# Optimization experiments

Hardware: AMD Instinct MI355X
Metric: run time of the kernel (lower is better)

## Reference

```python
import jax, jax.numpy as jnp
import numpy as np
import math

D_MODEL = 1024
NUM_HEADS = 16
HEAD_DIM = D_MODEL // NUM_HEADS  # 64
THETA = 10000.0
BATCH = 2
SEQ = 2048


def setup_inputs() -> dict:
    key = jax.random.key(0)
    ks = jax.random.split(key, 5)
    scale = 0.02
    return {
        "in_features": jax.random.normal(ks[0], (BATCH, SEQ, D_MODEL), jnp.float32),
        "q_proj": jax.random.normal(ks[1], (D_MODEL, D_MODEL), jnp.float32) * scale,
        "k_proj": jax.random.normal(ks[2], (D_MODEL, D_MODEL), jnp.float32) * scale,
        "v_proj": jax.random.normal(ks[3], (D_MODEL, D_MODEL), jnp.float32) * scale,
        "o_proj": jax.random.normal(ks[4], (D_MODEL, D_MODEL), jnp.float32) * scale,
        "token_positions": jnp.arange(SEQ, dtype=jnp.int32),
    }


def _rope(x, token_positions):
    # x: [b, h, s, head_dim]; interleaved even/odd rotation
    half = HEAD_DIM // 2
    inv_freq = 1.0 / (THETA ** (2.0 * jnp.arange(half, dtype=x.dtype) / HEAD_DIM))
    angle = token_positions.astype(x.dtype)[:, None] * inv_freq[None, :]  # [s, half]
    cos, sin = jnp.cos(angle), jnp.sin(angle)
    x_e, x_o = x[..., ::2], x[..., 1::2]
    r_e = x_e * cos - x_o * sin
    r_o = x_e * sin + x_o * cos
    # interleave back: [..., s, half, 2] -> [..., s, head_dim]
    return jnp.stack([r_e, r_o], axis=-1).reshape(x.shape)


def reference(in_features, q_proj, k_proj, v_proj, o_proj, token_positions):
    b, s, _ = in_features.shape
    # projections: weight layout is [d_out, d_in]
    Q = jnp.einsum('bsd,kd->bsk', in_features, q_proj)
    K = jnp.einsum('bsd,kd->bsk', in_features, k_proj)
    V = jnp.einsum('bsd,kd->bsk', in_features, v_proj)
    # split heads: [b, h, s, head_dim]
    Q = Q.reshape(b, s, NUM_HEADS, HEAD_DIM).transpose(0, 2, 1, 3)
    K = K.reshape(b, s, NUM_HEADS, HEAD_DIM).transpose(0, 2, 1, 3)
    V = V.reshape(b, s, NUM_HEADS, HEAD_DIM).transpose(0, 2, 1, 3)
    Q = _rope(Q, token_positions)
    K = _rope(K, token_positions)
    scores = jnp.einsum('bhnd,bhmd->bhnm', Q, K) / math.sqrt(HEAD_DIM)
    causal = jnp.tril(jnp.ones((s, s), dtype=bool))  # [s, s]
    scores = jnp.where(causal[None, None], scores, -jnp.inf)
    attn = jax.nn.softmax(scores, axis=-1)
    out = jnp.einsum('bhnm,bhmd->bhnd', attn, V)
    out = out.transpose(0, 2, 1, 3).reshape(b, s, D_MODEL)
    return jnp.einsum('bsv,dv->bsd', out, o_proj)
```

## Files before the change

### kernel.cpp

```cpp
#include <hip/hip_runtime.h>
#include <hip/hip_bf16.h>

#define D_MODEL 1024
#define NHEAD   16
#define HDIM    64
#define SEQQ    2048
#define NBATCH  2
#define MROWS   (NBATCH * SEQQ)

typedef unsigned short u16;
typedef __attribute__((ext_vector_type(8))) short short8;
typedef __attribute__((ext_vector_type(4))) short bf16x4;
typedef __attribute__((ext_vector_type(4))) float floatx4;

__device__ __forceinline__ u16 f2b(float f) {
    union { __hip_bfloat16 h; u16 u; } cv;
    cv.h = __float2bfloat16(f);
    return cv.u;
}
__device__ __forceinline__ float b2f(u16 u) {
    return __uint_as_float(((unsigned int)u) << 16);
}
__device__ __forceinline__ short8 load8(const u16* p) {
    return *reinterpret_cast<const short8*>(p);
}
__device__ __forceinline__ bf16x4 load4v(const u16* p) {
    return *reinterpret_cast<const bf16x4*>(p);
}
__device__ __forceinline__ unsigned pack2(float lo, float hi) {
    return ((unsigned)f2b(hi) << 16) | (unsigned)f2b(lo);
}
__device__ __forceinline__ void async_cp16(const void* g, void* l) {
    __builtin_amdgcn_global_load_lds(
        (const __attribute__((address_space(1))) void*)g,
        (__attribute__((address_space(3))) void*)l, 16, 0, 0);
}

__global__ void cvt_all(const float* __restrict__ X,
                        const float* __restrict__ w0, const float* __restrict__ w1,
                        const float* __restrict__ w2, const float* __restrict__ w3,
                        const int* __restrict__ pos,
                        u16* __restrict__ xo,
                        u16* __restrict__ o0, u16* __restrict__ o1,
                        u16* __restrict__ o2, u16* __restrict__ o3,
                        float2* __restrict__ tab) {
    const int z = blockIdx.y;
    if (z == 8) {
        const int i = blockIdx.x * 256 + threadIdx.x;
        if (i < SEQQ * 32) {
            const int s = i >> 5, j = i & 31;
            const float p = (float)pos[s];
            const float inv = expf(-(float)j * (9.210340371976184f / 32.0f));
            float sn, cs;
            sincosf(p * inv, &sn, &cs);
            tab[i] = make_float2(cs, sn);
        }
        return;
    }
    const int n4 = (D_MODEL * D_MODEL) / 4;
    const float* in;
    u16* out;
    if (z < 4) { in = X + (size_t)z * n4 * 4;  out = xo + (size_t)z * n4 * 4; }
    else {
        in  = (z == 4) ? w0 : (z == 5) ? w1 : (z == 6) ? w2 : w3;
        out = (z == 4) ? o0 : (z == 5) ? o1 : (z == 6) ? o2 : o3;
    }
    const int i = blockIdx.x * 256 + threadIdx.x;
    float4 v = reinterpret_cast<const float4*>(in)[i];
    ushort4 o;
    o.x = f2b(v.x); o.y = f2b(v.y); o.z = f2b(v.z); o.w = f2b(v.w);
    reinterpret_cast<ushort4*>(out)[i] = o;
}

__global__ __launch_bounds__(256) void gemm_qkv(
    const u16* __restrict__ A,
    const u16* __restrict__ B0, const u16* __restrict__ B1, const u16* __restrict__ B2,
    u16* __restrict__ Qt, u16* __restrict__ Kt, u16* __restrict__ Vt,
    const float2* __restrict__ tab)
{
    const int K = D_MODEL;
    const int z = blockIdx.z;
    const u16* Bt = (z == 0) ? B0 : (z == 1 ? B1 : B2);

    __shared__ __attribute__((aligned(16))) u16 As[128 * 32];
    __shared__ __attribute__((aligned(16))) u16 Bs[128 * 32];

    const int tid  = threadIdx.x;
    const int w    = tid >> 6;
    const int lane = tid & 63;
    const int l15  = lane & 15;
    const int quad = lane >> 4;
    const int wm   = w >> 1, wn = w & 1;
    const int tm   = blockIdx.x * 128, tn = blockIdx.y * 128;

    floatx4 acc[4][4];
#pragma unroll
    for (int i = 0; i < 4; i++)
#pragma unroll
        for (int j = 0; j < 4; j++) {
            floatx4 zz = {0.f, 0.f, 0.f, 0.f};
            acc[i][j] = zz;
        }

    const int srow = lane >> 2;
    const int scol = (lane & 3) * 8;

    for (int k0 = 0; k0 < K; k0 += 32) {
#pragma unroll
        for (int ch = w; ch < 8; ch += 4) {
            async_cp16(A  + (size_t)(tm + ch * 16 + srow) * K + k0 + scol, &As[ch * 512]);
            async_cp16(Bt + (size_t)(tn + ch * 16 + srow) * K + k0 + scol, &Bs[ch * 512]);
        }
        __syncthreads();

        short8 af[4], bfr[4];
#pragma unroll
        for (int mi = 0; mi < 4; mi++)
            af[mi] = load8(&As[(wm * 64 + mi * 16 + l15) * 32 + quad * 8]);
#pragma unroll
        for (int ni = 0; ni < 4; ni++)
            bfr[ni] = load8(&Bs[(wn * 64 + ni * 16 + l15) * 32 + quad * 8]);
#pragma unroll
        for (int mi = 0; mi < 4; mi++)
#pragma unroll
            for (int ni = 0; ni < 4; ni++)
                acc[mi][ni] = __builtin_amdgcn_mfma_f32_16x16x32_bf16(af[mi], bfr[ni], acc[mi][ni], 0, 0, 0);
        __syncthreads();
    }

    if (z == 2) {
#pragma unroll
        for (int mi = 0; mi < 4; mi++) {
            const int r0 = tm + wm * 64 + mi * 16 + quad * 4;
            const int bb = r0 >> 11, s0 = r0 & (SEQQ - 1);
#pragma unroll
            for (int ni = 0; ni < 4; ni++) {
                const int colb = tn + wn * 64 + ni * 16 + l15;
                const int d = colb & 63, hh = colb >> 6;
                ushort4 pk;
                pk.x = f2b(acc[mi][ni][0]);
                pk.y = f2b(acc[mi][ni][1]);
                pk.z = f2b(acc[mi][ni][2]);
                pk.w = f2b(acc[mi][ni][3]);
                *reinterpret_cast<ushort4*>(
                    &Vt[(((size_t)(bb * NHEAD + hh)) * HDIM + d) * SEQQ + s0]) = pk;
            }
        }
    } else {
        const float qsc = (z == 0) ? 0.18033688011112042f : 1.0f;
        u16* Outp = (z == 0) ? Qt : Kt;
#pragma unroll
        for (int mi = 0; mi < 4; mi++) {
            const int r0 = tm + wm * 64 + mi * 16 + quad * 4;
#pragma unroll
            for (int ni = 0; ni < 4; ni++) {
                const int colb = tn + wn * 64 + ni * 16 + l15;
                const int d = colb & 63, hh = colb >> 6;
                const int j = d >> 1;
                const bool odd = (d & 1) != 0;
#pragma unroll
                for (int rg = 0; rg < 4; rg++) {
                    const int r = r0 + rg;
                    const int bb = r >> 11, s = r & (SEQQ - 1);
                    const float own = acc[mi][ni][rg];
                    const float oth = __shfl_xor(own, 1);
                    const float2 cs = tab[s * 32 + j];
                    const float xe = odd ? oth : own;
                    const float xo = odd ? own : oth;
                    const float res = odd ? (xe * cs.y + xo * cs.x)
                                          : (xe * cs.x - xo * cs.y);
                    Outp[(((size_t)(bb * NHEAD + hh)) * SEQQ + s) * HDIM + d] =
                        f2b(res * qsc);
                }
            }
        }
    }
}

__global__ __launch_bounds__(256, 4) void attn_kernel(
    const u16* __restrict__ Qt, const u16* __restrict__ Kt, const u16* __restrict__ Vt,
    u16* __restrict__ Out)
{
    const int bid = blockIdx.x;
    const int xcd = bid & 7;
    const int u   = bid >> 3;
    const int col = xcd * 4 + (u & 3);
    const int m   = u >> 2;
    int qsub;
    if      (m < 8)  qsub = 31 - m;
    else if (m < 16) qsub = m - 8;
    else if (m < 24) qsub = 39 - m;
    else             qsub = m - 16;
    const int h = col & (NHEAD - 1), b = col >> 4;

    const int tid = threadIdx.x, w = tid >> 6, lane = tid & 63;
    const int l15 = lane & 15, quad = lane >> 4;
    const size_t bh = (size_t)(b * NHEAD + h);
    const u16* Qh = Qt + bh * SEQQ * HDIM;
    const u16* Kh = Kt + bh * SEQQ * HDIM;
    const u16* Vh = Vt + bh * HDIM * SEQQ;

    __shared__ __attribute__((aligned(16))) u16 Ks[2][64 * 64];
    __shared__ __attribute__((aligned(16))) u16 Vs[2][64 * 64];

    short8 ones;
#pragma unroll
    for (int i = 0; i < 8; i++) ones[i] = (short)0x3F80;

    const int rr  = lane >> 3;
    const int swz = ((lane & 7) ^ rr) * 8;
    auto stage = [&](int buf, int tt) {
        const int k0s = tt * 64;
        async_cp16(Kh + (size_t)(k0s + w * 8 + rr) * HDIM + swz,       &Ks[buf][w * 512]);
        async_cp16(Kh + (size_t)(k0s + (w + 4) * 8 + rr) * HDIM + swz, &Ks[buf][(w + 4) * 512]);
        async_cp16(Vh + (size_t)(w * 8 + rr) * SEQQ + k0s + swz,       &Vs[buf][w * 512]);
        async_cp16(Vh + (size_t)((w + 4) * 8 + rr) * SEQQ + k0s + swz, &Vs[buf][(w + 4) * 512]);
    };

    const int s7  = l15 & 7;
    const int sw1 = ((quad)     ^ s7) * 8;
    const int sw2 = ((quad + 4) ^ s7) * 8;
    const int vo0 = (((quad >> 1)    ) ^ s7) * 8 + (quad & 1) * 4;
    const int vo1 = (((quad >> 1) + 2) ^ s7) * 8 + (quad & 1) * 4;
    const int vo2 = (((quad >> 1) + 4) ^ s7) * 8 + (quad & 1) * 4;
    const int vo3 = (((quad >> 1) + 6) ^ s7) * 8 + (quad & 1) * 4;

    const int q0w   = qsub * 64 + w * 16;
    const int tmaxp = qsub;

    short8 qf[2];
#pragma unroll
    for (int kk = 0; kk < 2; kk++)
        qf[kk] = load8(&Qh[(size_t)(q0w + l15) * HDIM + kk * 32 + quad * 8]);

    floatx4 O[4];
    floatx4 l_acc = {0.f, 0.f, 0.f, 0.f};
#pragma unroll
    for (int c = 0; c < 4; c++) { floatx4 zz = {0.f, 0.f, 0.f, 0.f}; O[c] = zz; }

    stage(0, 0);

    for (int t = 0; t <= tmaxp; ++t) {
        asm volatile("s_waitcnt vmcnt(0)" ::: "memory");
        __builtin_amdgcn_s_barrier();
        if (t < tmaxp) stage((t + 1) & 1, t + 1);

        const u16* KsB = &Ks[t & 1][0];
        const u16* VsB = &Vs[t & 1][0];
        const int k0 = t * 64;

        floatx4 S[4];
#pragma unroll
        for (int c = 0; c < 4; c++) {
            const int rowb = (c * 16 + l15) * 64;
            floatx4 zz = {0.f, 0.f, 0.f, 0.f};
            S[c] = __builtin_amdgcn_mfma_f32_16x16x32_bf16(load8(&KsB[rowb + sw1]), qf[0], zz,   0, 0, 0);
            S[c] = __builtin_amdgcn_mfma_f32_16x16x32_bf16(load8(&KsB[rowb + sw2]), qf[1], S[c], 0, 0, 0);
        }

        if (t == tmaxp) {
            const int q = q0w + l15;
#pragma unroll
            for (int c = 0; c < 4; c++)
#pragma unroll
                for (int r = 0; r < 4; r++)
                    if (k0 + c * 16 + quad * 4 + r > q) S[c][r] = -1e30f;
        }

#pragma unroll
        for (int c = 0; c < 4; c++)
#pragma unroll
            for (int r = 0; r < 4; r++)
                S[c][r] = __builtin_amdgcn_exp2f(S[c][r]);

        union { short8 v; unsigned u[4]; } pf0, pf1;
        pf0.u[0] = pack2(S[0][0], S[0][1]);
        pf0.u[1] = pack2(S[0][2], S[0][3]);
        pf0.u[2] = pack2(S[1][0], S[1][1]);
        pf0.u[3] = pack2(S[1][2], S[1][3]);
        pf1.u[0] = pack2(S[2][0], S[2][1]);
        pf1.u[1] = pack2(S[2][2], S[2][3]);
        pf1.u[2] = pack2(S[3][0], S[3][1]);
        pf1.u[3] = pack2(S[3][2], S[3][3]);

        l_acc = __builtin_amdgcn_mfma_f32_16x16x32_bf16(pf0.v, ones, l_acc, 0, 0, 0);
        l_acc = __builtin_amdgcn_mfma_f32_16x16x32_bf16(pf1.v, ones, l_acc, 0, 0, 0);

#pragma unroll
        for (int c2 = 0; c2 < 4; c2++) {
            const int rowb = (c2 * 16 + l15) * 64;
            bf16x4 a0 = load4v(&VsB[rowb + vo0]);
            bf16x4 a1 = load4v(&VsB[rowb + vo1]);
            bf16x4 a2 = load4v(&VsB[rowb + vo2]);
            bf16x4 a3 = load4v(&VsB[rowb + vo3]);
            short8 v0 = __builtin_shufflevector(a0, a1, 0, 1, 2, 3, 4, 5, 6, 7);
            short8 v1 = __builtin_shufflevector(a2, a3, 0, 1, 2, 3, 4, 5, 6, 7);
            O[c2] = __builtin_amdgcn_mfma_f32_16x16x32_bf16(pf0.v, v0, O[c2], 0, 0, 0);
            O[c2] = __builtin_amdgcn_mfma_f32_16x16x32_bf16(pf1.v, v1, O[c2], 0, 0, 0);
        }
    }

    float inv_l[4];
#pragma unroll
    for (int r = 0; r < 4; r++) inv_l[r] = 1.0f / l_acc[r];

#pragma unroll
    for (int c2 = 0; c2 < 4; c2++)
#pragma unroll
        for (int r = 0; r < 4; r++) {
            const int q    = q0w + quad * 4 + r;
            const int colo = h * HDIM + c2 * 16 + l15;
            Out[(size_t)(b * SEQQ + q) * D_MODEL + colo] = f2b(O[c2][r] * inv_l[r]);
        }
}

__global__ __launch_bounds__(256) void gemm_o(
    const u16* __restrict__ A, const u16* __restrict__ Bt, float* __restrict__ C)
{
    const int K = D_MODEL, N = D_MODEL;
    __shared__ __attribute__((aligned(16))) u16 As[64 * 32];
    __shared__ __attribute__((aligned(16))) u16 Bs[128 * 32];

    const int tid  = threadIdx.x;
    const int w    = tid >> 6;
    const int lane = tid & 63;
    const int l15  = lane & 15;
    const int quad = lane >> 4;
    const int wm   = w >> 1, wn = w & 1;
    const int tm   = blockIdx.x * 64, tn = blockIdx.y * 128;

    floatx4 acc[2][4];
#pragma unroll
    for (int i = 0; i < 2; i++)
#pragma unroll
        for (int j = 0; j < 4; j++) {
            floatx4 z = {0.f, 0.f, 0.f, 0.f};
            acc[i][j] = z;
        }

    const int srow = lane >> 2;
    const int scol = (lane & 3) * 8;

    for (int k0 = 0; k0 < K; k0 += 32) {
#pragma unroll
        for (int ch = w; ch < 12; ch += 4) {
            if (ch < 4) async_cp16(A  + (size_t)(tm + ch * 16 + srow) * K + k0 + scol, &As[ch * 512]);
            else        async_cp16(Bt + (size_t)(tn + (ch - 4) * 16 + srow) * K + k0 + scol, &Bs[(ch - 4) * 512]);
        }
        __syncthreads();

        short8 af[2], bfr[4];
#pragma unroll
        for (int mi = 0; mi < 2; mi++)
            af[mi] = load8(&As[(wm * 32 + mi * 16 + l15) * 32 + quad * 8]);
#pragma unroll
        for (int ni = 0; ni < 4; ni++)
            bfr[ni] = load8(&Bs[(wn * 64 + ni * 16 + l15) * 32 + quad * 8]);
#pragma unroll
        for (int mi = 0; mi < 2; mi++)
#pragma unroll
            for (int ni = 0; ni < 4; ni++)
                acc[mi][ni] = __builtin_amdgcn_mfma_f32_16x16x32_bf16(af[mi], bfr[ni], acc[mi][ni], 0, 0, 0);
        __syncthreads();
    }

#pragma unroll
    for (int mi = 0; mi < 2; mi++)
#pragma unroll
        for (int ni = 0; ni < 4; ni++)
#pragma unroll
            for (int rg = 0; rg < 4; rg++) {
                int row = tm + wm * 32 + mi * 16 + quad * 4 + rg;
                int col = tn + wn * 64 + ni * 16 + l15;
                C[(size_t)row * N + col] = acc[mi][ni][rg];
            }
}

extern "C" void kernel_launch(void* const* d_in, const int* in_sizes, int n_in,
                              void* d_out, int out_size, void* d_ws, size_t ws_size,
                              hipStream_t stream)
{
    const float* X  = (const float*)d_in[0];
    const float* Wq = (const float*)d_in[1];
    const float* Wk = (const float*)d_in[2];
    const float* Wv = (const float*)d_in[3];
    const float* Wo = (const float*)d_in[4];
    const int* tpos = (const int*)d_in[5];
    float* out = (float*)d_out;
    char* ws = (char*)d_ws;

    const size_t MB = (size_t)1 << 20;
    u16*    Xb  = (u16*)(ws + 0);
    u16*    WqB = (u16*)(ws + 8 * MB);
    u16*    WkB = (u16*)(ws + 10 * MB);
    u16*    WvB = (u16*)(ws + 12 * MB);
    u16*    WoB = (u16*)(ws + 14 * MB);
    float2* tab = (float2*)(ws + 16 * MB);
    u16*    Qt  = (u16*)(ws + 24 * MB);
    u16*    Kt  = (u16*)(ws + 32 * MB);
    u16*    Vt  = (u16*)(ws + 40 * MB);
    u16*   AOut = (u16*)(ws + 48 * MB);

    cvt_all<<<dim3(1024, 9), 256, 0, stream>>>(X, Wq, Wk, Wv, Wo, tpos,
                                               Xb, WqB, WkB, WvB, WoB, tab);

    gemm_qkv<<<dim3(32, 8, 3), 256, 0, stream>>>(Xb, WqB, WkB, WvB,
                                                 Qt, Kt, Vt, tab);
    attn_kernel<<<dim3(1024, 1, 1), 256, 0, stream>>>(Qt, Kt, Vt, AOut);
    gemm_o<<<dim3(64, 8), 256, 0, stream>>>(AOut, WoB, out);
}
```

Measured before the change: 190.0 us.

## Double-buffer GEMM LDS tiles and de-interleave Q/K weights for vectorized RoPE

Both projection GEMMs get double-buffered LDS staging, so the async global-to-LDS copy of the next K tile overlaps the MFMA work on the current tile, using raw barriers and vmcnt waits. The Q/K weight rows are permuted during the bf16 conversion so even and odd RoPE dimensions land in separate column halves. This lets the epilogue pair accumulators within a thread instead of using cross-lane shuffles. The cos/sin table is transposed to [j][s] so each thread can read consecutive positions with float4 loads. The cost is twice the LDS per block, which may lower occupancy, plus the Q/K stores in the epilogue become scattered 2-byte writes.

Result: faster. 186.3 us (-2.0%).

```diff
diff --git a/kernel.cpp b/kernel.cpp
--- a/kernel.cpp
+++ b/kernel.cpp
@@ -45,10 +45,10 @@
                         u16* __restrict__ o2, u16* __restrict__ o3,
                         float2* __restrict__ tab) {
     const int z = blockIdx.y;
+    const int i = blockIdx.x * 256 + threadIdx.x;
     if (z == 8) {
-        const int i = blockIdx.x * 256 + threadIdx.x;
         if (i < SEQQ * 32) {
-            const int s = i >> 5, j = i & 31;
+            const int j = i >> 11, s = i & (SEQQ - 1);
             const float p = (float)pos[s];
             const float inv = expf(-(float)j * (9.210340371976184f / 32.0f));
             float sn, cs;
@@ -65,8 +65,14 @@
         in  = (z == 4) ? w0 : (z == 5) ? w1 : (z == 6) ? w2 : w3;
         out = (z == 4) ? o0 : (z == 5) ? o1 : (z == 6) ? o2 : o3;
     }
-    const int i = blockIdx.x * 256 + threadIdx.x;
-    float4 v = reinterpret_cast<const float4*>(in)[i];
+    int src = i;
+    if (z == 4 || z == 5) {
+        const int orow = i >> 8;
+        const int g    = i & 255;
+        const int irow = (orow & ~63) | (((orow & 31) << 1) | ((orow >> 5) & 1));
+        src = irow * 256 + g;
+    }
+    float4 v = reinterpret_cast<const float4*>(in)[src];
     ushort4 o;
     o.x = f2b(v.x); o.y = f2b(v.y); o.z = f2b(v.z); o.w = f2b(v.w);
     reinterpret_cast<ushort4*>(out)[i] = o;
@@ -82,8 +88,8 @@
     const int z = blockIdx.z;
     const u16* Bt = (z == 0) ? B0 : (z == 1 ? B1 : B2);
 
-    __shared__ __attribute__((aligned(16))) u16 As[128 * 32];
-    __shared__ __attribute__((aligned(16))) u16 Bs[128 * 32];
+    __shared__ __attribute__((aligned(16))) u16 As[2][128 * 32];
+    __shared__ __attribute__((aligned(16))) u16 Bs[2][128 * 32];
 
     const int tid  = threadIdx.x;
     const int w    = tid >> 6;
@@ -105,27 +111,37 @@
     const int srow = lane >> 2;
     const int scol = (lane & 3) * 8;
 
-    for (int k0 = 0; k0 < K; k0 += 32) {
+    auto stage = [&](int buf, int k0) {
 #pragma unroll
         for (int ch = w; ch < 8; ch += 4) {
-            async_cp16(A  + (size_t)(tm + ch * 16 + srow) * K + k0 + scol, &As[ch * 512]);
-            async_cp16(Bt + (size_t)(tn + ch * 16 + srow) * K + k0 + scol, &Bs[ch * 512]);
-        }
-        __syncthreads();
+            async_cp16(A  + (size_t)(tm + ch * 16 + srow) * K + k0 + scol, &As[buf][ch * 512]);
+            async_cp16(Bt + (size_t)(tn + ch * 16 + srow) * K + k0 + scol, &Bs[buf][ch * 512]);
+        }
+    };
+
+    stage(0, 0);
+
+    for (int kt = 0; kt < 32; ++kt) {
+        asm volatile("s_waitcnt vmcnt(0)" ::: "memory");
+        __builtin_amdgcn_s_barrier();
+        if (kt < 31) stage((kt + 1) & 1, (kt + 1) * 32);
+
+        const u16* AsB = &As[kt & 1][0];
+        const u16* BsB = &Bs[kt & 1][0];
 
         short8 af[4], bfr[4];
 #pragma unroll
         for (int mi = 0; mi < 4; mi++)
-            af[mi] = load8(&As[(wm * 64 + mi * 16 + l15) * 32 + quad * 8]);
+            af[mi] = load8(&AsB[(wm * 64 + mi * 16 + l15) * 32 + quad * 8]);
 #pragma unroll
         for (int ni = 0; ni < 4; ni++)
-            bfr[ni] = load8(&Bs[(wn * 64 + ni * 16 + l15) * 32 + quad * 8]);
+            bfr[ni] = load8(&BsB[(wn * 64 + ni * 16 + l15) * 32 + quad * 8]);
 #pragma unroll
         for (int mi = 0; mi < 4; mi++)
 #pragma unroll
             for (int ni = 0; ni < 4; ni++)
                 acc[mi][ni] = __builtin_amdgcn_mfma_f32_16x16x32_bf16(af[mi], bfr[ni], acc[mi][ni], 0, 0, 0);
-        __syncthreads();
+        __builtin_amdgcn_s_barrier();
     }
 
     if (z == 2) {
@@ -152,25 +168,26 @@
 #pragma unroll
         for (int mi = 0; mi < 4; mi++) {
             const int r0 = tm + wm * 64 + mi * 16 + quad * 4;
-#pragma unroll
-            for (int ni = 0; ni < 4; ni++) {
-                const int colb = tn + wn * 64 + ni * 16 + l15;
-                const int d = colb & 63, hh = colb >> 6;
-                const int j = d >> 1;
-                const bool odd = (d & 1) != 0;
+            const int bb = r0 >> 11, s0 = r0 & (SEQQ - 1);
+#pragma unroll
+            for (int ni = 0; ni < 2; ni++) {
+                const int p_e = tn + wn * 64 + ni * 16 + l15;
+                const int hh = p_e >> 6;
+                const int qq = p_e & 63;
+                const float4 t01 = *reinterpret_cast<const float4*>(&tab[qq * SEQQ + s0]);
+                const float4 t23 = *reinterpret_cast<const float4*>(&tab[qq * SEQQ + s0 + 2]);
+                const float cs[4] = {t01.x, t01.z, t23.x, t23.z};
+                const float sn[4] = {t01.y, t01.w, t23.y, t23.w};
 #pragma unroll
                 for (int rg = 0; rg < 4; rg++) {
-                    const int r = r0 + rg;
-                    const int bb = r >> 11, s = r & (SEQQ - 1);
-                    const float own = acc[mi][ni][rg];
-                    const float oth = __shfl_xor(own, 1);
-                    const float2 cs = tab[s * 32 + j];
-                    const float xe = odd ? oth : own;
-                    const float xo = odd ? own : oth;
-                    const float res = odd ? (xe * cs.y + xo * cs.x)
-                                          : (xe * cs.x - xo * cs.y);
-                    Outp[(((size_t)(bb * NHEAD + hh)) * SEQQ + s) * HDIM + d] =
-                        f2b(res * qsc);
+                    const float e = acc[mi][ni][rg];
+                    const float o = acc[mi][ni + 2][rg];
+                    const float re = (e * cs[rg] - o * sn[rg]) * qsc;
+                    const float ro = (e * sn[rg] + o * cs[rg]) * qsc;
+                    const size_t base =
+                        (((size_t)(bb * NHEAD + hh)) * SEQQ + (s0 + rg)) * HDIM;
+                    Outp[base + qq]      = f2b(re);
+                    Outp[base + 32 + qq] = f2b(ro);
                 }
             }
         }
@@ -318,8 +335,8 @@
     const u16* __restrict__ A, const u16* __restrict__ Bt, float* __restrict__ C)
 {
     const int K = D_MODEL, N = D_MODEL;
-    __shared__ __attribute__((aligned(16))) u16 As[64 * 32];
-    __shared__ __attribute__((aligned(16))) u16 Bs[128 * 32];
+    __shared__ __attribute__((aligned(16))) u16 As[2][64 * 32];
+    __shared__ __attribute__((aligned(16))) u16 Bs[2][128 * 32];
 
     const int tid  = threadIdx.x;
     const int w    = tid >> 6;
@@ -341,27 +358,37 @@
     const int srow = lane >> 2;
     const int scol = (lane & 3) * 8;
 
-    for (int k0 = 0; k0 < K; k0 += 32) {
+    auto stage = [&](int buf, int k0) {
 #pragma unroll
         for (int ch = w; ch < 12; ch += 4) {
-            if (ch < 4) async_cp16(A  + (size_t)(tm + ch * 16 + srow) * K + k0 + scol, &As[ch * 512]);
-            else        async_cp16(Bt + (size_t)(tn + (ch - 4) * 16 + srow) * K + k0 + scol, &Bs[(ch - 4) * 512]);
-        }
-        __syncthreads();
+            if (ch < 4) async_cp16(A  + (size_t)(tm + ch * 16 + srow) * K + k0 + scol, &As[buf][ch * 512]);
+            else        async_cp16(Bt + (size_t)(tn + (ch - 4) * 16 + srow) * K + k0 + scol, &Bs[buf][(ch - 4) * 512]);
+        }
+    };
+
+    stage(0, 0);
+
+    for (int kt = 0; kt < 32; ++kt) {
+        asm volatile("s_waitcnt vmcnt(0)" ::: "memory");
+        __builtin_amdgcn_s_barrier();
+        if (kt < 31) stage((kt + 1) & 1, (kt + 1) * 32);
+
+        const u16* AsB = &As[kt & 1][0];
+        const u16* BsB = &Bs[kt & 1][0];
 
         short8 af[2], bfr[4];
 #pragma unroll
         for (int mi = 0; mi < 2; mi++)
-            af[mi] = load8(&As[(wm * 32 + mi * 16 + l15) * 32 + quad * 8]);
+            af[mi] = load8(&AsB[(wm * 32 + mi * 16 + l15) * 32 + quad * 8]);
 #pragma unroll
         for (int ni = 0; ni < 4; ni++)
-            bfr[ni] = load8(&Bs[(wn * 64 + ni * 16 + l15) * 32 + quad * 8]);
+            bfr[ni] = load8(&BsB[(wn * 64 + ni * 16 + l15) * 32 + quad * 8]);
 #pragma unroll
         for (int mi = 0; mi < 2; mi++)
 #pragma unroll
             for (int ni = 0; ni < 4; ni++)
                 acc[mi][ni] = __builtin_amdgcn_mfma_f32_16x16x32_bf16(af[mi], bfr[ni], acc[mi][ni], 0, 0, 0);
-        __syncthreads();
+        __builtin_amdgcn_s_barrier();
     }
 
 #pragma unroll
```
